# Optimization experiments

Measured on AMD Instinct MI355X. Metric: run time of the kernel, lower is better.

## Reference

```python
import jax, jax.numpy as jnp
import numpy as np

THRESHOLD = 0.95
MAX_LABELS = 64  # static pad length; alphas rows sum to 64 so fire count <= 64


def setup_inputs() -> dict:
    key = jax.random.key(0)
    k1, k2 = jax.random.split(key)
    B, T, H = 32, 2000, 512
    hidden = jax.random.normal(k1, (B, T, H), dtype=jnp.float32)
    raw = jax.random.uniform(k2, (B, T), minval=0.1, maxval=1.0, dtype=jnp.float32)
    # mimic forward(): alpha *= num / alpha.sum(-1), with num = 64 labels per utt
    alphas = raw * (64.0 / raw.sum(-1, keepdims=True))
    return {"hidden": hidden, "alphas": alphas}


def _cif(hidden, alphas, threshold):
    """Continuous integrate-and-fire: sequential threshold-reset scan over time,
    then gather fired frames into a padded [B, MAX_LABELS, H] tensor."""
    B, T, H = hidden.shape

    def step(carry, xs):
        integrate, frame = carry          # [B], [B,H]
        h_t, a_t = xs                     # [B,H], [B]
        dist_completion = 1.0 - integrate
        integrate = integrate + a_t
        fire = integrate > threshold
        fire_val = integrate              # recorded pre-reset (torch list_fires)
        integrate = jnp.where(fire, integrate - 1.0, integrate)
        cur = jnp.where(fire, dist_completion, a_t)
        frame_out = frame + cur[:, None] * h_t   # recorded (torch list_frames)
        remainds = a_t - cur
        frame = jnp.where(fire[:, None], remainds[:, None] * h_t, frame_out)
        return (integrate, frame), (fire_val, frame_out)

    init = (jnp.zeros((B,), hidden.dtype), jnp.zeros((B, H), hidden.dtype))
    _, (fires, frames) = jax.lax.scan(
        step, init, (hidden.transpose(1, 0, 2), alphas.T))
    fires = fires.T                    # [B,T]
    frames = frames.transpose(1, 0, 2) # [B,T,H]

    # extract fired frames in order, pad to MAX_LABELS (vectorized scatter)
    fired = fires > threshold          # [B,T] bool
    pos = jnp.where(fired, jnp.cumsum(fired, axis=1) - 1, MAX_LABELS)
    out = jnp.zeros((B, MAX_LABELS + 1, H), hidden.dtype)
    out = out.at[jnp.arange(B)[:, None], pos].set(frames)
    return out[:, :MAX_LABELS]  # drop the dump slot


def reference(hidden, alphas):
    return _cif(hidden, alphas, THRESHOLD)
```

## Files before the change

kernel.cpp:

```cpp
#include <hip/hip_runtime.h>

#define THRESH 0.95f
#define MAXL 64
#define RSTR 65

__device__ __forceinline__ float rlane(float v, int lane) {
    return __uint_as_float(__builtin_amdgcn_readlane(__float_as_uint(v), lane));
}

__global__ __launch_bounds__(64) void cif_scan(
    const float* __restrict__ alphas, int T, int B,
    int* __restrict__ nf, uint2* __restrict__ recs) {
    int b = blockIdx.x;
    if (b >= B) return;
    int lane = threadIdx.x;
    const float* arow = alphas + (size_t)b * T;
    uint2* rec = recs + (size_t)b * RSTR;

    float integ = 0.0f;
    unsigned n = 0;
    int nwin = T >> 3;
    bool fast = ((((uintptr_t)arow) & 15) == 0) && (nwin > 0);

    if (fast) {
        const float4* g4 = (const float4*)arow;
        int ngrp = (nwin + 63) >> 6;
        float4 z = make_float4(0.f, 0.f, 0.f, 0.f);
        float4 pa = z, pb = z, qa = z, qb = z;
        if (lane < nwin) { pa = g4[lane * 2]; pb = g4[lane * 2 + 1]; }
        for (int j = 0; j < ngrp; ++j) {
            int wbase = j << 6;
            int lim = nwin - wbase; if (lim > 64) lim = 64;
            if (j + 1 < ngrp) {
                int nx = wbase + 64 + lane;
                qa = z; qb = z;
                if (nx < nwin) { qa = g4[nx * 2]; qb = g4[nx * 2 + 1]; }
            }
            unsigned sg = __float_as_uint(pa.x) | __float_as_uint(pa.y) |
                          __float_as_uint(pa.z) | __float_as_uint(pa.w) |
                          __float_as_uint(pb.x) | __float_as_uint(pb.y) |
                          __float_as_uint(pb.z) | __float_as_uint(pb.w);
            bool gneg = __ballot((sg >> 31) & 1u) != 0ull;

            for (int w2 = 0; w2 < lim; ++w2) {
                float c0 = rlane(pa.x, w2), c1 = rlane(pa.y, w2);
                float c2 = rlane(pa.z, w2), c3 = rlane(pa.w, w2);
                float c4 = rlane(pb.x, w2), c5 = rlane(pb.y, w2);
                float c6 = rlane(pb.z, w2), c7 = rlane(pb.w, w2);
                float s1 = integ + c0, s2 = s1 + c1;
                float s3 = s2 + c2,    s4 = s3 + c3;
                float s5 = s4 + c4,    s6 = s5 + c5;
                float s7 = s6 + c6,    s8 = s7 + c7;
                if (__builtin_expect((s8 > THRESH) || gneg, 0)) {
                    int tb = (wbase + w2) << 3;
                    float cur = integ;
                    float vv[8] = {c0, c1, c2, c3, c4, c5, c6, c7};
                    #pragma unroll
                    for (int ii = 0; ii < 8; ++ii) {
                        float p = cur;
                        float x = p + vv[ii];
                        if (x > THRESH) {
                            if (n < MAXL)
                                rec[n] = make_uint2(__float_as_uint(p),
                                                    (unsigned)(tb + ii));
                            ++n;
                            x = x - 1.0f;
                        }
                        cur = x;
                    }
                    integ = cur;
                } else {
                    integ = s8;
                }
            }
            pa = qa; pb = qb;
        }
    }
    int tstart = fast ? (nwin << 3) : 0;
    for (int t = tstart; t < T; ++t) {
        float p = integ;
        float x = p + arow[t];
        if (x > THRESH) {
            if (n < MAXL) rec[n] = make_uint2(__float_as_uint(p), (unsigned)t);
            ++n;
            x = x - 1.0f;
        }
        integ = x;
    }
    nf[b] = (n < MAXL) ? (int)n : MAXL;
}

__global__ __launch_bounds__(128) void cif_gather(
    const float* __restrict__ hidden, const float* __restrict__ alphas,
    int T, int H,
    const int* __restrict__ nf, const uint2* __restrict__ recs,
    float* __restrict__ out) {
    int b = blockIdx.x >> 6;
    int k = blockIdx.x & (MAXL - 1);

    int valid = (k < nf[b]);
    int tf = 0, t0 = 0, tp = 0;
    float rw = 0.0f, cw = 0.0f;
    const float* arow = alphas + (size_t)b * T;
    if (valid) {
        uint2 r = recs[(size_t)b * RSTR + k];
        cw = 1.0f - __uint_as_float(r.x);
        tf = (int)r.y;
        if (k > 0) {
            uint2 rp = recs[(size_t)b * RSTR + k - 1];
            tp = (int)rp.y;
            float dcp = 1.0f - __uint_as_float(rp.x);
            rw = arow[tp] - dcp;
            t0 = tp + 1;
        }
    }

    if ((H & 3) == 0) {
        int W = H >> 2;
        const float4* hb4 = (const float4*)(hidden + (size_t)b * T * H);
        float4* out4 = (float4*)(out + (size_t)blockIdx.x * H);
        for (int h4 = threadIdx.x; h4 < W; h4 += blockDim.x) {
            float4 acc = make_float4(0.f, 0.f, 0.f, 0.f);
            if (valid) {
                if (k > 0) {
                    float4 m = hb4[(size_t)tp * W + h4];
                    acc.x = rw * m.x; acc.y = rw * m.y;
                    acc.z = rw * m.z; acc.w = rw * m.w;
                }
                for (int t = t0; t < tf; ++t) {
                    float4 m = hb4[(size_t)t * W + h4];
                    float a = arow[t];
                    acc.x += a * m.x; acc.y += a * m.y;
                    acc.z += a * m.z; acc.w += a * m.w;
                }
                float4 m = hb4[(size_t)tf * W + h4];
                acc.x += cw * m.x; acc.y += cw * m.y;
                acc.z += cw * m.z; acc.w += cw * m.w;
            }
            out4[h4] = acc;
        }
    } else {
        const float* hb = hidden + (size_t)b * T * H;
        size_t obase = (size_t)blockIdx.x * H;
        for (int h = threadIdx.x; h < H; h += blockDim.x) {
            float acc = 0.0f;
            if (valid) {
                if (k > 0) acc = rw * hb[(size_t)tp * H + h];
                for (int t = t0; t < tf; ++t)
                    acc += arow[t] * hb[(size_t)t * H + h];
                acc += cw * hb[(size_t)tf * H + h];
            }
            out[obase + h] = acc;
        }
    }
}

extern "C" void kernel_launch(void* const* d_in, const int* in_sizes, int n_in,
                              void* d_out, int out_size, void* d_ws, size_t ws_size,
                              hipStream_t stream) {
    const float* hidden = (const float*)d_in[0];
    const float* alphas = (const float*)d_in[1];
    float* out = (float*)d_out;

    long BT  = in_sizes[1];
    long BTH = in_sizes[0];
    int H = (int)(BTH / BT);
    int B = (int)((long)out_size / ((long)MAXL * H));
    int T = (int)(BT / B);

    char* ws = (char*)d_ws;
    int*   nf   = (int*)ws;
    uint2* recs = (uint2*)(ws + 256);

    cif_scan<<<B, 64, 0, stream>>>(alphas, T, B, nf, recs);
    cif_gather<<<B * MAXL, 128, 0, stream>>>(hidden, alphas, T, H, nf, recs, out);
}
```

Baseline: 60.22 us.

## Pack scan waves into blocks and buffer fire records in registers

The scan kernel now runs 16 independent waves per block, one batch row per wave, instead of one 64-thread block per row. Fire records are kept in lane registers, with lane n holding the n-th fire, and written out together at the end instead of through scattered single-lane stores inside the loop. Branch conditions are made wave-uniform with ballots. The intent is to cut store latency and divergence on the serial scan's critical path. The cost is extra ballot and select instructions per fire step.

```diff
diff --git a/kernel.cpp b/kernel.cpp
--- a/kernel.cpp
+++ b/kernel.cpp
@@ -3,25 +3,42 @@
 #define THRESH 0.95f
 #define MAXL 64
 #define RSTR 65
+#define WVB  16
 
 __device__ __forceinline__ float rlane(float v, int lane) {
     return __uint_as_float(__builtin_amdgcn_readlane(__float_as_uint(v), lane));
 }
 
-__global__ __launch_bounds__(64) void cif_scan(
+__global__ __launch_bounds__(1024, 4) void cif_scan(
     const float* __restrict__ alphas, int T, int B,
     int* __restrict__ nf, uint2* __restrict__ recs) {
-    int b = blockIdx.x;
+    int wv   = threadIdx.x >> 6;
+    int lane = threadIdx.x & 63;
+    int b = blockIdx.x * WVB + wv;
     if (b >= B) return;
-    int lane = threadIdx.x;
     const float* arow = alphas + (size_t)b * T;
     uint2* rec = recs + (size_t)b * RSTR;
 
     float integ = 0.0f;
-    unsigned n = 0;
+    int n = 0;
+    unsigned vpre = 0u, vt = 0u;
+
+#define FSTEP(CV, TT)                                                        \
+    {                                                                        \
+        float p = cur;                                                       \
+        float x = p + (CV);                                                  \
+        bool f = x > THRESH;                                                 \
+        cur = f ? (x - 1.0f) : x;                                            \
+        if (__ballot(f) != 0ull) {        \
+            bool sel = (lane == n) & (n < MAXL);                             \
+            vpre = sel ? __float_as_uint(p) : vpre;                          \
+            vt   = sel ? (unsigned)(TT)     : vt;                            \
+            ++n;                                                             \
+        }                                                                    \
+    }
+
     int nwin = T >> 3;
-    bool fast = ((((uintptr_t)arow) & 15) == 0) && (nwin > 0);
-
+    bool fast = ((((uintptr_t)arow) & 15) == 0) && (nwin >= 1);
     if (fast) {
         const float4* g4 = (const float4*)arow;
         int ngrp = (nwin + 63) >> 6;
@@ -40,7 +57,7 @@
                           __float_as_uint(pa.z) | __float_as_uint(pa.w) |
                           __float_as_uint(pb.x) | __float_as_uint(pb.y) |
                           __float_as_uint(pb.z) | __float_as_uint(pb.w);
-            bool gneg = __ballot((sg >> 31) & 1u) != 0ull;
+            bool gneg = __ballot(((sg >> 31) & 1u) != 0u) != 0ull;
 
             for (int w2 = 0; w2 < lim; ++w2) {
                 float c0 = rlane(pa.x, w2), c1 = rlane(pa.y, w2);
@@ -51,23 +68,14 @@
                 float s3 = s2 + c2,    s4 = s3 + c3;
                 float s5 = s4 + c4,    s6 = s5 + c5;
                 float s7 = s6 + c6,    s8 = s7 + c7;
-                if (__builtin_expect((s8 > THRESH) || gneg, 0)) {
+                bool trig = (s8 > THRESH) | gneg;
+                if (__ballot(trig) != 0ull) {
                     int tb = (wbase + w2) << 3;
                     float cur = integ;
-                    float vv[8] = {c0, c1, c2, c3, c4, c5, c6, c7};
-                    #pragma unroll
-                    for (int ii = 0; ii < 8; ++ii) {
-                        float p = cur;
-                        float x = p + vv[ii];
-                        if (x > THRESH) {
-                            if (n < MAXL)
-                                rec[n] = make_uint2(__float_as_uint(p),
-                                                    (unsigned)(tb + ii));
-                            ++n;
-                            x = x - 1.0f;
-                        }
-                        cur = x;
-                    }
+                    FSTEP(c0, tb)     FSTEP(c1, tb + 1)
+                    FSTEP(c2, tb + 2) FSTEP(c3, tb + 3)
+                    FSTEP(c4, tb + 4) FSTEP(c5, tb + 5)
+                    FSTEP(c6, tb + 6) FSTEP(c7, tb + 7)
                     integ = cur;
                 } else {
                     integ = s8;
@@ -76,18 +84,19 @@
             pa = qa; pb = qb;
         }
     }
-    int tstart = fast ? (nwin << 3) : 0;
-    for (int t = tstart; t < T; ++t) {
-        float p = integ;
-        float x = p + arow[t];
-        if (x > THRESH) {
-            if (n < MAXL) rec[n] = make_uint2(__float_as_uint(p), (unsigned)t);
-            ++n;
-            x = x - 1.0f;
+    {
+        float cur = integ;
+        for (int t = fast ? (nwin << 3) : 0; t < T; ++t) {
+            float a = arow[t];
+            FSTEP(a, t)
         }
-        integ = x;
+        integ = cur;
     }
-    nf[b] = (n < MAXL) ? (int)n : MAXL;
+#undef FSTEP
+
+    int nfb = (n < MAXL) ? n : MAXL;
+    if (lane < nfb) rec[lane] = make_uint2(vpre, vt);
+    if (lane == 0) nf[b] = nfb;
 }
 
 __global__ __launch_bounds__(128) void cif_gather(
@@ -172,6 +181,7 @@
     int*   nf   = (int*)ws;
     uint2* recs = (uint2*)(ws + 256);
 
-    cif_scan<<<B, 64, 0, stream>>>(alphas, T, B, nf, recs);
+    int nblk = (B + WVB - 1) / WVB;
+    cif_scan<<<nblk, WVB * 64, 0, stream>>>(alphas, T, B, nf, recs);
     cif_gather<<<B * MAXL, 128, 0, stream>>>(hidden, alphas, T, H, nf, recs, out);
 }
```

Result: slower. 103.6 us (+72.1%).
